# Kernel tuning notes

Measured on AMD Instinct MI355X. Metric: run time of the kernel, lower is better.

The kernel has to match this reference:

```python
import jax, jax.numpy as jnp
import numpy as np
from jax.scipy.special import gammaln

INTERVAL_STEPS = (1, -1, -3, 3, 4, -4)
MARGIN = 0.5


def _build_transition(S):
    # T[f, t, i] = 1 if t == f + interval_steps[i], else 0 (within support)
    T = np.zeros((S, S, len(INTERVAL_STEPS)), dtype=np.float32)
    for i, s in enumerate(INTERVAL_STEPS):
        if s > 0:
            f = np.arange(0, S - s)
        else:
            f = np.arange(-s, S)
        T[f, f + s, i] = 1.0
    return jnp.asarray(T)


def _forward(data, log_weights):
    n_data, C = data.shape
    S = int(np.ceil((2 * MARGIN + 1) * C))              # n_dist_support = 256
    center = int(np.round((MARGIN + 0.5) * C))           # reference_center = 128
    down = -min(min(INTERVAL_STEPS), 0)
    up = max(max(INTERVAL_STEPS), 0)
    n_iters = int(np.ceil(max(center / down, (S - center) / up))) + 1  # 33
    T = _build_transition(S)

    # Poisson-weighted Markov diffusion
    w = jnp.exp(log_weights)
    rate = w.sum(axis=1)                                 # [d]
    p = w / rate[:, None]                                # [d, i] interval step probs
    log_rate = jnp.log(rate)
    run0 = jnp.zeros((n_data, S), data.dtype).at[:, center].set(1.0)
    acc0 = jnp.zeros((n_data, S), data.dtype)

    def diff_step(carry, n):
        acc, run = carry
        step_prob = jnp.exp(n * log_rate - rate - gammaln(n + 1.0))  # Poisson pmf(n)
        acc = acc + step_prob[:, None] * run
        # einsum('fti,di,df->dt') done as two controlled contractions
        tmp = jnp.einsum('fti,df->dti', T, run)          # [d, t, i]
        run = jnp.einsum('dti,di->dt', tmp, p)           # [d, t]
        return (acc, run), None

    (acc, _), _ = jax.lax.scan(diff_step, (acc0, run0),
                               jnp.arange(n_iters, dtype=data.dtype))
    icd = acc / acc.sum(axis=1, keepdims=True)           # [d, S]

    # match distributions: min over shifts of DKL(data || normalized slice)
    n_shifts = S - C + 1
    pz = jnp.isclose(data, 0.0)
    safe_p = jnp.where(pz, 1.0, data)
    plogp = jnp.where(pz, 0.0, data * jnp.log(safe_p))   # [d, C]

    def match_step(carry, shift):
        best_loss, best_dist = carry
        d = jax.lax.dynamic_slice_in_dim(icd, shift, C, axis=1)
        d = d / d.sum(axis=1, keepdims=True)
        logq = jnp.log(jnp.maximum(d, 1e-38))            # guard fp32 underflow at edges
        loss = (plogp - jnp.where(pz, 0.0, data * logq)).sum(axis=1)
        cond = loss < best_loss
        return (jnp.where(cond, loss, best_loss),
                jnp.where(cond[:, None], d, best_dist)), None

    init = (jnp.full((n_data,), jnp.inf, data.dtype), jnp.zeros_like(data))
    (matched_loss, matched_dist), _ = jax.lax.scan(match_step, init, jnp.arange(n_shifts))
    return matched_loss


def setup_inputs() -> dict:
    key = jax.random.key(0)
    k1, k2 = jax.random.split(key)
    u = jax.random.uniform(k1, (4096, 128), jnp.float32)
    data = u / u.sum(axis=1, keepdims=True)              # rows are distributions
    # small weights -> Poisson rates ~6, so cum prob is allclose(1) before iter 33,
    # matching the original module's break-at-effective_min_iterations behavior
    log_weights = 0.1 * jax.random.normal(k2, (4096, 6), jnp.float32)
    return {"data": data, "log_weights": log_weights}


def reference(data, log_weights):
    return _forward(data, log_weights)
```

## Files before the change

### kernel.cpp

```cpp
#include <hip/hip_runtime.h>
#include <math.h>

#define NC      128
#define NSTATE  256
#define NITERS  33
#define NSTEPS  6
#define RPB     4
#define LN2     (0.6931471805599453f)

#define DPP_WAVE_SHL1 0x130
#define DPP_WAVE_SHR1 0x138

__device__ __forceinline__ float dpp_shr1(float x) {
    return __int_as_float(__builtin_amdgcn_update_dpp(
        0, __float_as_int(x), DPP_WAVE_SHR1, 0xf, 0xf, true));
}
__device__ __forceinline__ float dpp_shl1(float x) {
    return __int_as_float(__builtin_amdgcn_update_dpp(
        0, __float_as_int(x), DPP_WAVE_SHL1, 0xf, 0xf, true));
}

__global__ __launch_bounds__(256, 4)
void tonal_diffusion_kernel(const float* __restrict__ data,
                            const float* __restrict__ logw,
                            float* __restrict__ out, int n_rows)
{
    const int wid  = threadIdx.x >> 6;
    const int lane = threadIdx.x & 63;
    int row = blockIdx.x * RPB + wid;
    row = row < n_rows ? row : n_rows - 1;
    const int urow = __builtin_amdgcn_readfirstlane(row);

    __shared__ __align__(16) float licdR_s[RPB][4][NSTATE];
    __shared__ __align__(16) float P_s    [RPB][NSTATE];
    float (* __restrict__ licdR)[NSTATE] = licdR_s[wid];
    float * __restrict__ P               = P_s[wid];

    const float* __restrict__ drow = data + (size_t)urow * NC;

    float rate, p0, p1, p2, p3, p4, p5;
    {
        const float* lw = logw + urow * NSTEPS;
        p0 = __expf(lw[0]); p1 = __expf(lw[1]); p2 = __expf(lw[2]);
        p3 = __expf(lw[3]); p4 = __expf(lw[4]); p5 = __expf(lw[5]);
        rate = ((p0 + p1) + (p2 + p3)) + (p4 + p5);
        const float inv = 1.0f / rate;
        p0 *= inv; p1 *= inv; p2 *= inv; p3 *= inv; p4 *= inv; p5 *= inv;
    }

    const float2 dl = *(const float2*)(drow + 2 * lane);
    float plogp;
    {
        float pl = 0.f;
        if (dl.x > 1e-8f) pl += dl.x * __logf(dl.x);
        if (dl.y > 1e-8f) pl += dl.y * __logf(dl.y);
        #pragma unroll
        for (int off = 1; off < 64; off <<= 1) pl += __shfl_xor(pl, off, 64);
        plogp = pl;
    }

    float r0 = 0.f, r1 = 0.f, r2 = 0.f, r3 = 0.f;
    if (lane == 32) r0 = 1.0f;
    float a0 = 0.f, a1 = 0.f, a2 = 0.f, a3 = 0.f;
    float sp = __expf(-rate);
    #pragma unroll
    for (int n = 0; n < NITERS; ++n) {
        a0 += sp * r0; a1 += sp * r1; a2 += sp * r2; a3 += sp * r3;
        const float L0 = dpp_shr1(r0), L1 = dpp_shr1(r1),
                    L2 = dpp_shr1(r2), L3 = dpp_shr1(r3);
        const float R0 = dpp_shl1(r0), R1 = dpp_shl1(r1),
                    R2 = dpp_shl1(r2), R3 = dpp_shl1(r3);
        const float n0 = p0*L3 + p1*r1 + p2*r3 + p3*L1 + p4*L0 + p5*R0;
        const float n1 = p0*r0 + p1*r2 + p2*R0 + p3*L2 + p4*L1 + p5*R1;
        const float n2 = p0*r1 + p1*r3 + p2*R1 + p3*L3 + p4*L2 + p5*R2;
        const float n3 = p0*r2 + p1*R0 + p2*R2 + p3*r0 + p4*L3 + p5*R3;
        r0 = n0; r1 = n1; r2 = n2; r3 = n3;
        sp = sp * rate * (1.0f / (float)(n + 1));
    }

    {
        const float l0 = __log2f(a0), l1 = __log2f(a1),
                    l2 = __log2f(a2), l3 = __log2f(a3);
        const float nl0 = dpp_shl1(l0), nl1 = dpp_shl1(l1), nl2 = dpp_shl1(l2);
        *(float4*)&licdR[0][4 * lane] = make_float4(l0, l1, l2, l3);
        *(float4*)&licdR[1][4 * lane] = make_float4(l1, l2, l3, nl0);
        *(float4*)&licdR[2][4 * lane] = make_float4(l2, l3, nl0, nl1);
        *(float4*)&licdR[3][4 * lane] = make_float4(l3, nl0, nl1, nl2);
    }

    {
        const float s0 = a0, s1 = s0 + a1, s2 = s1 + a2, s3 = s2 + a3;
        float t = s3;
        #pragma unroll
        for (int off = 1; off < 64; off <<= 1) {
            const float u = __shfl_up(t, off, 64);
            if (lane >= off) t += u;
        }
        const float base = t - s3;
        *(float4*)&P[4 * lane] = make_float4(base + s0, base + s1, base + s2, base + s3);
    }

    const int phi = lane & 3;
    const float* __restrict__ lcp = &licdR[phi][lane - phi];
    const float zA2 = __log2f(P[lane + 127] - (lane ? P[lane - 1] : 0.f));
    const float zB2 = __log2f(P[lane + 191] - P[lane + 63]);
    float dotA = 0.f, dotB = 0.f;
    #pragma unroll 4
    for (int j = 0; j < 16; ++j) {
        const float4 L1v = *(const float4*)(lcp + 4 * j);
        const float4 L2v = *(const float4*)(lcp + 4 * j + 64);
        const float4 L3v = *(const float4*)(lcp + 4 * j + 128);
        const float4 dLo = *(const float4*)(drow + 4 * j);
        const float4 dHi = *(const float4*)(drow + 4 * j + 64);
        dotA += dLo.x * L1v.x; dotA += dLo.y * L1v.y;
        dotA += dLo.z * L1v.z; dotA += dLo.w * L1v.w;
        dotA += dHi.x * L2v.x; dotA += dHi.y * L2v.y;
        dotA += dHi.z * L2v.z; dotA += dHi.w * L2v.w;
        dotB += dLo.x * L2v.x; dotB += dLo.y * L2v.y;
        dotB += dLo.z * L2v.z; dotB += dLo.w * L2v.w;
        dotB += dHi.x * L3v.x; dotB += dHi.y * L3v.y;
        dotB += dHi.z * L3v.z; dotB += dHi.w * L3v.w;
    }
    float best2 = fminf(zA2 - dotA, zB2 - dotB);

    {
        const float z2 = __log2f(P[255] - P[127]);
        const float2 lv = *(const float2*)(&licdR[0][128 + 2 * lane]);
        float part = dl.x * lv.x + dl.y * lv.y;
        #pragma unroll
        for (int off = 1; off < 64; off <<= 1) part += __shfl_xor(part, off, 64);
        best2 = fminf(best2, z2 - part);
    }

    #pragma unroll
    for (int off = 1; off < 64; off <<= 1) best2 = fminf(best2, __shfl_xor(best2, off, 64));
    if (lane == 0) out[row] = plogp + LN2 * best2;
}

extern "C" void kernel_launch(void* const* d_in, const int* in_sizes, int n_in,
                              void* d_out, int out_size, void* d_ws, size_t ws_size,
                              hipStream_t stream)
{
    const float* data = (const float*)d_in[0];
    const float* logw = (const float*)d_in[1];
    float* out = (float*)d_out;
    const int n_rows = in_sizes[0] / NC;
    const int blocks = (n_rows + RPB - 1) / RPB;
    tonal_diffusion_kernel<<<blocks, 256, 0, stream>>>(data, logw, out, n_rows);
}
```

Measured before the change: 72.23 us.

## Split match-phase dot products across two waves per row

Assigns two waves to each row, with each wave redundantly running the full diffusion but computing only half of the shift-matching dot products (A or B). The halves are combined through shared memory after a block barrier, and the launch-bounds occupancy hint is raised. This shortens the serial match phase per wave but doubles the diffusion work per row and the number of waves, and adds a __syncthreads.

```diff
diff --git a/kernel.cpp b/kernel.cpp
--- a/kernel.cpp
+++ b/kernel.cpp
@@ -5,7 +5,7 @@
 #define NSTATE  256
 #define NITERS  33
 #define NSTEPS  6
-#define RPB     4
+#define RPB     2
 #define LN2     (0.6931471805599453f)
 
 #define DPP_WAVE_SHL1 0x130
@@ -20,19 +20,23 @@
         0, __float_as_int(x), DPP_WAVE_SHL1, 0xf, 0xf, true));
 }
 
-__global__ __launch_bounds__(256, 4)
+__global__ __launch_bounds__(256, 8)
 void tonal_diffusion_kernel(const float* __restrict__ data,
                             const float* __restrict__ logw,
                             float* __restrict__ out, int n_rows)
 {
-    const int wid  = threadIdx.x >> 6;
-    const int lane = threadIdx.x & 63;
-    int row = blockIdx.x * RPB + wid;
+    const int tid  = threadIdx.x;
+    const int wid  = tid >> 6;
+    const int lane = tid & 63;
+    const int rib  = wid >> 1;
+    const int h    = wid & 1;
+    int row = blockIdx.x * RPB + rib;
     row = row < n_rows ? row : n_rows - 1;
     const int urow = __builtin_amdgcn_readfirstlane(row);
 
-    __shared__ __align__(16) float licdR_s[RPB][4][NSTATE];
-    __shared__ __align__(16) float P_s    [RPB][NSTATE];
+    __shared__ __align__(16) float licdR_s[4][4][NSTATE];
+    __shared__ __align__(16) float P_s    [4][NSTATE];
+    __shared__ float red_s[RPB][2];
     float (* __restrict__ licdR)[NSTATE] = licdR_s[wid];
     float * __restrict__ P               = P_s[wid];
 
@@ -102,39 +106,51 @@
 
     const int phi = lane & 3;
     const float* __restrict__ lcp = &licdR[phi][lane - phi];
-    const float zA2 = __log2f(P[lane + 127] - (lane ? P[lane - 1] : 0.f));
-    const float zB2 = __log2f(P[lane + 191] - P[lane + 63]);
-    float dotA = 0.f, dotB = 0.f;
-    #pragma unroll 4
-    for (int j = 0; j < 16; ++j) {
-        const float4 L1v = *(const float4*)(lcp + 4 * j);
-        const float4 L2v = *(const float4*)(lcp + 4 * j + 64);
-        const float4 L3v = *(const float4*)(lcp + 4 * j + 128);
-        const float4 dLo = *(const float4*)(drow + 4 * j);
-        const float4 dHi = *(const float4*)(drow + 4 * j + 64);
-        dotA += dLo.x * L1v.x; dotA += dLo.y * L1v.y;
-        dotA += dLo.z * L1v.z; dotA += dLo.w * L1v.w;
-        dotA += dHi.x * L2v.x; dotA += dHi.y * L2v.y;
-        dotA += dHi.z * L2v.z; dotA += dHi.w * L2v.w;
-        dotB += dLo.x * L2v.x; dotB += dLo.y * L2v.y;
-        dotB += dLo.z * L2v.z; dotB += dLo.w * L2v.w;
-        dotB += dHi.x * L3v.x; dotB += dHi.y * L3v.y;
-        dotB += dHi.z * L3v.z; dotB += dHi.w * L3v.w;
-    }
-    float best2 = fminf(zA2 - dotA, zB2 - dotB);
-
-    {
+    float best2;
+    if (h == 0) {
+        const float zA2 = __log2f(P[lane + 127] - (lane ? P[lane - 1] : 0.f));
+        float dotA = 0.f;
+        #pragma unroll 2
+        for (int j = 0; j < 16; ++j) {
+            const float4 L1v = *(const float4*)(lcp + 4 * j);
+            const float4 L2v = *(const float4*)(lcp + 4 * j + 64);
+            const float4 dLo = *(const float4*)(drow + 4 * j);
+            const float4 dHi = *(const float4*)(drow + 4 * j + 64);
+            dotA += dLo.x * L1v.x; dotA += dLo.y * L1v.y;
+            dotA += dLo.z * L1v.z; dotA += dLo.w * L1v.w;
+            dotA += dHi.x * L2v.x; dotA += dHi.y * L2v.y;
+            dotA += dHi.z * L2v.z; dotA += dHi.w * L2v.w;
+        }
+        best2 = zA2 - dotA;
         const float z2 = __log2f(P[255] - P[127]);
         const float2 lv = *(const float2*)(&licdR[0][128 + 2 * lane]);
         float part = dl.x * lv.x + dl.y * lv.y;
         #pragma unroll
         for (int off = 1; off < 64; off <<= 1) part += __shfl_xor(part, off, 64);
         best2 = fminf(best2, z2 - part);
+    } else {
+        const float zB2 = __log2f(P[lane + 191] - P[lane + 63]);
+        float dotB = 0.f;
+        #pragma unroll 2
+        for (int j = 0; j < 16; ++j) {
+            const float4 L2v = *(const float4*)(lcp + 4 * j + 64);
+            const float4 L3v = *(const float4*)(lcp + 4 * j + 128);
+            const float4 dLo = *(const float4*)(drow + 4 * j);
+            const float4 dHi = *(const float4*)(drow + 4 * j + 64);
+            dotB += dLo.x * L2v.x; dotB += dLo.y * L2v.y;
+            dotB += dLo.z * L2v.z; dotB += dLo.w * L2v.w;
+            dotB += dHi.x * L3v.x; dotB += dHi.y * L3v.y;
+            dotB += dHi.z * L3v.z; dotB += dHi.w * L3v.w;
+        }
+        best2 = zB2 - dotB;
     }
 
     #pragma unroll
     for (int off = 1; off < 64; off <<= 1) best2 = fminf(best2, __shfl_xor(best2, off, 64));
-    if (lane == 0) out[row] = plogp + LN2 * best2;
+    if (lane == 0) red_s[rib][h] = best2;
+    __syncthreads();
+    if (lane == 0 && h == 0)
+        out[row] = plogp + LN2 * fminf(red_s[rib][0], red_s[rib][1]);
 }
 
 extern "C" void kernel_launch(void* const* d_in, const int* in_sizes, int n_in,
```

New measurement: 86.78 us. +20.1%, slower.
